# Performance work log

Hardware: AMD Instinct MI355X
Metric: run time of the kernel (lower is better)

The kernel has to match this reference:

```python
import jax, jax.numpy as jnp
import numpy as np

NIBBLES_PER_I32 = 8


def unpack_int4(q):
    """Unpack int32 [..., n] -> uint4 values in int32 [..., n*8], LSB-first."""
    shifts = (jnp.arange(NIBBLES_PER_I32, dtype=jnp.int32) * 4)
    nib = (q[..., None] >> shifts) & 0xF  # [..., n, 8]
    return nib.reshape(q.shape[:-1] + (q.shape[-1] * NIBBLES_PER_I32,))


def setup_inputs() -> dict:
    key = jax.random.key(0)
    k_x, k_w, k_z, k_s, k_b = jax.random.split(key, 5)
    B, S, IN, OUT, G = 2, 4096, 4096, 4096, 32
    x = jax.random.normal(k_x, (B, S, IN), dtype=jnp.float16)
    qweight = jax.random.randint(k_w, (OUT, IN // 8), 0, 2147483647, dtype=jnp.int32)
    qzeros = jax.random.randint(k_z, (G, OUT // 8), 0, 2147483647, dtype=jnp.int32)
    scales = (jax.random.uniform(k_s, (G, OUT), dtype=jnp.float32) * 0.01 + 0.001).astype(jnp.float16)
    bias = (jax.random.normal(k_b, (OUT,), dtype=jnp.float32) * 0.01).astype(jnp.float16)
    return {"x": x, "qweight": qweight, "qzeros": qzeros, "scales": scales, "bias": bias}


def reference(x, qweight, qzeros, scales, bias):
    # GPTQ W4A16: dequantize int4 weight with per-group scales/zero-points, then GEMM + bias.
    x = x.astype(jnp.float16)
    wq = unpack_int4(qweight)            # [out, in] int4 values
    zq = unpack_int4(qzeros)             # [groups, out]
    out_f, in_f = wq.shape
    G = scales.shape[0]
    gsize = in_f // G
    wq_g = wq.reshape(out_f, G, gsize)                       # [out, G, gsize]
    zero = zq.T.astype(jnp.float16)[:, :, None]              # [out, G, 1]
    scale = scales.T.astype(jnp.float16)[:, :, None]         # [out, G, 1]
    w = ((wq_g.astype(jnp.float16) - zero) * scale).reshape(out_f, in_f)  # [out, in] fp16
    y = jnp.einsum("bsi,oi->bso", x, w)                     # [B, S, out]
    return y + bias
```

## Files before the change

kernel.cpp:

```cpp
#include <hip/hip_runtime.h>
#include <cstdint>

typedef unsigned short u16;
typedef unsigned int   u32;
typedef unsigned long long u64;

typedef _Float16 f16x2 __attribute__((ext_vector_type(2)));
typedef _Float16 f16x8 __attribute__((ext_vector_type(8)));
typedef float    f32x4 __attribute__((ext_vector_type(4)));

__device__ __forceinline__ u32 cvt_pk(float a, float b) {
    return __builtin_bit_cast(u32, __builtin_amdgcn_cvt_pkrtz(a, b));
}

__device__ __forceinline__ f16x8 unpack_dq(u32 q, f16x2 cz, f16x2 cs) {
    const u32 b0 = (q & 0x000F000Fu) | 0x64006400u;
    const u32 b1 = ((q >> 4) & 0x000F000Fu) | 0x64006400u;
    const u32 b2 = ((q >> 8) & 0x000F000Fu) | 0x64006400u;
    const u32 b3 = ((q >> 12) & 0x000F000Fu) | 0x64006400u;
    const f16x2 w0 = (__builtin_bit_cast(f16x2, b0) - cz) * cs;
    const f16x2 w1 = (__builtin_bit_cast(f16x2, b1) - cz) * cs;
    const f16x2 w2 = (__builtin_bit_cast(f16x2, b2) - cz) * cs;
    const f16x2 w3 = (__builtin_bit_cast(f16x2, b3) - cz) * cs;
    uint4 w;
    w.x = __builtin_bit_cast(u32, w0);
    w.y = __builtin_bit_cast(u32, w1);
    w.z = __builtin_bit_cast(u32, w2);
    w.w = __builtin_bit_cast(u32, w3);
    return __builtin_bit_cast(f16x8, w);
}

__device__ __forceinline__ void load_lds16(const void* g, void* l) {
    __builtin_amdgcn_global_load_lds(
        (const __attribute__((address_space(1))) void*)g,
        (__attribute__((address_space(3))) void*)l,
        16, 0, 0);
}

__global__ __launch_bounds__(256) void gptq_prepass(
    const float* __restrict__ X, u16* __restrict__ Xh)
{
    const u32 tile = blockIdx.x;
    const u32 mt = tile >> 6, t = tile & 63;
    const float* bsrc = X + ((u64)mt << 19) + t * 64;
    u16* bdst = Xh + ((u64)tile << 13);
#pragma unroll
    for (int pass = 0; pass < 4; ++pass) {
        const u32 idx = pass * 256 + threadIdx.x;
        const u32 r = idx >> 3, sg = idx & 7, g = sg ^ (r & 7);
        const float* s = bsrc + ((u64)r << 12) + g * 8;
        const float4 f0 = *(const float4*)s;
        const float4 f1 = *(const float4*)(s + 4);
        uint4 w;
        w.x = cvt_pk(f0.x, f1.x);
        w.y = cvt_pk(f0.y, f1.y);
        w.z = cvt_pk(f0.z, f1.z);
        w.w = cvt_pk(f0.w, f1.w);
        *(uint4*)(bdst + idx * 8) = w;
    }
}

__global__ __launch_bounds__(256) void gptq_dequantB(
    const int* __restrict__ QW, const int* __restrict__ QZ,
    const float* __restrict__ SC, u16* __restrict__ Bt)
{
    __shared__ int tile[64][65];
    const u32 bkq = blockIdx.x;
    const u32 bn  = blockIdx.y;
    const u32 t = threadIdx.x;
    const u32 r = t >> 4, c4 = (t & 15) * 4;
#pragma unroll
    for (int p = 0; p < 4; ++p) {
        const u32 row = p * 16 + r;
        const int4 v = *(const int4*)(QW + (u64)(bn * 64 + row) * 512
                                         + bkq * 64 + c4);
        tile[row][c4 + 0] = v.x; tile[row][c4 + 1] = v.y;
        tile[row][c4 + 2] = v.z; tile[row][c4 + 3] = v.w;
    }
    __syncthreads();
    char* BtB = (char*)Bt;
#pragma unroll
    for (int p = 0; p < 4; ++p) {
        const u32 kql = p * 16 + r;
        const u32 chunk = bkq * 64 + kql;
        const u32 g = chunk >> 4;
        const u32 quad = chunk & 3;
        const u64 base = ((u64)((chunk >> 2) * 256)) * 1024 + quad * 256;
#pragma unroll
        for (int e = 0; e < 4; ++e) {
            const u32 n = bn * 64 + c4 + e;
            const u32 q = (u32)tile[c4 + e][kql];
            const float s = SC[g * 4096 + n];
            const int zw = QZ[g * 512 + (n >> 3)];
            const int z = (zw >> ((n & 7) * 4)) & 0xF;
            const _Float16 hs = (_Float16)s;
            const _Float16 hz = (_Float16)(float)(1024 + z);
            const f16x8 v = unpack_dq(q, (f16x2){hz, hz}, (f16x2){hs, hs});
            *(f16x8*)(BtB + base + (u64)(n >> 4) * 1024 + (n & 15) * 16) = v;
        }
    }
}

__global__ __launch_bounds__(256, 2) void gptq_gemm_dq(
    const u16* __restrict__ Xh,
    const u16* __restrict__ Bt,
    const float* __restrict__ BIAS,
    float* __restrict__ Y)
{
    constexpr int N = 4096, NT = 64;

    __shared__ __align__(16) u16 Alds[2][128 * 64];

    const int tid  = threadIdx.x;
    const int lane = tid & 63;
    const int wid  = tid >> 6;

    const int mt = blockIdx.x;
    const int m0 = mt * 128;
    const int n0 = blockIdx.y * 256;

    f32x4 acc[8][4];
#pragma unroll
    for (int i = 0; i < 8; i++)
#pragma unroll
        for (int j = 0; j < 4; j++)
            acc[i][j] = (f32x4){0.f, 0.f, 0.f, 0.f};

    const int fr   = lane & 15;
    const int quad = lane >> 4;
    const int fr7  = fr & 7;

    const char* xsrc = (const char*)Xh + (((u64)mt * NT) << 14)
                     + wid * 4096 + lane * 16;

    const int nb16 = (n0 >> 4) + wid * 4;
    const char* btb = (const char*)Bt + (u64)nb16 * 1024 + lane * 16;

    f16x8 bq[2][2][4];

    auto STAGE = [&](int buf, int t) {
        const char* s = xsrc + ((u64)t << 14);
        char* d = (char*)&Alds[buf][0] + wid * 4096;
#pragma unroll
        for (int i = 0; i < 4; i++)
            load_lds16(s + i * 1024, d + i * 1024);
    };

    auto FETCH_B = [&](int t, int nb) {
#pragma unroll
        for (int ks = 0; ks < 2; ks++) {
            const char* p = btb + ((u64)(t * 2 + ks) << 18);
#pragma unroll
            for (int ni = 0; ni < 4; ni++)
                bq[nb][ks][ni] = *(const f16x8*)(p + ni * 1024);
        }
    };

    auto COMPUTE = [&](int buf, int nb) {
#pragma unroll
        for (int ks = 0; ks < 2; ks++) {
            const int gsw = ((ks * 4 + quad) ^ fr7) * 8;
            __builtin_amdgcn_s_setprio(1);
#pragma unroll
            for (int mi = 0; mi < 8; mi++) {
                const f16x8 af =
                    *(const f16x8*)(&Alds[buf][(mi * 16 + fr) * 64 + gsw]);
#pragma unroll
                for (int ni = 0; ni < 4; ni++)
                    acc[mi][ni] = __builtin_amdgcn_mfma_f32_16x16x32_f16(
                        af, bq[nb][ks][ni], acc[mi][ni], 0, 0, 0);
            }
            __builtin_amdgcn_s_setprio(0);
        }
    };

    FETCH_B(0, 0);
    STAGE(0, 0);
    STAGE(1, 1);
    asm volatile("s_waitcnt vmcnt(4)\n\ts_barrier" ::: "memory");

    for (int t = 0; t <= 60; t += 2) {
        FETCH_B(t + 1, 1);
        COMPUTE(0, 0);
        asm volatile("s_barrier" ::: "memory");
        STAGE(0, t + 2);
        asm volatile("s_waitcnt vmcnt(12)\n\ts_barrier" ::: "memory");

        FETCH_B(t + 2, 0);
        COMPUTE(1, 1);
        asm volatile("s_barrier" ::: "memory");
        STAGE(1, t + 3);
        asm volatile("s_waitcnt vmcnt(12)\n\ts_barrier" ::: "memory");
    }

    FETCH_B(63, 1);
    COMPUTE(0, 0);
    asm volatile("s_waitcnt vmcnt(8)\n\ts_barrier" ::: "memory");
    COMPUTE(1, 1);

    const int cn  = lane & 15;
    const int q4r = quad * 4;
#pragma unroll
    for (int ni = 0; ni < 4; ni++) {
        const int col = n0 + wid * 64 + ni * 16 + cn;
        const float bz = BIAS[col];
#pragma unroll
        for (int mi = 0; mi < 8; mi++) {
            const int rbase = m0 + mi * 16 + q4r;
#pragma unroll
            for (int r = 0; r < 4; r++) {
                Y[(u64)(rbase + r) * N + col] = acc[mi][ni][r] + bz;
            }
        }
    }
}

__global__ __launch_bounds__(256) void gptq_transpose(
    const int* __restrict__ QW, int* __restrict__ QWt)
{
    __shared__ int tile[64][65];
    const u32 bkq = blockIdx.x, bn = blockIdx.y;
    const u32 t = threadIdx.x;
    const u32 r = t >> 4, c4 = (t & 15) * 4;
#pragma unroll
    for (int p = 0; p < 4; ++p) {
        const u32 row = p * 16 + r;
        const int4 v = *(const int4*)(QW + (u64)(bn * 64 + row) * 512
                                         + bkq * 64 + c4);
        tile[row][c4 + 0] = v.x; tile[row][c4 + 1] = v.y;
        tile[row][c4 + 2] = v.z; tile[row][c4 + 3] = v.w;
    }
    __syncthreads();
#pragma unroll
    for (int p = 0; p < 4; ++p) {
        const u32 kql = p * 16 + r;
        int4 v;
        v.x = tile[c4 + 0][kql]; v.y = tile[c4 + 1][kql];
        v.z = tile[c4 + 2][kql]; v.w = tile[c4 + 3][kql];
        *(int4*)(QWt + (u64)(bkq * 64 + kql) * 4096 + bn * 64 + c4) = v;
    }
}

__global__ __launch_bounds__(256, 2) void gptq_gemm_dma(
    const u16* __restrict__ Xh, const int* __restrict__ QWt,
    const int* __restrict__ QZ, const float* __restrict__ SC,
    const float* __restrict__ BIAS, float* __restrict__ Y)
{
    constexpr int N = 4096, NT = 64;
    __shared__ __align__(16) u16 Alds[2][128 * 64];
    const int tid = threadIdx.x, lane = tid & 63, wid = tid >> 6;
    const int mt = blockIdx.x, m0 = mt * 128, n0 = blockIdx.y * 256;
    f32x4 acc[8][4];
#pragma unroll
    for (int i = 0; i < 8; i++)
#pragma unroll
        for (int j = 0; j < 4; j++) acc[i][j] = (f32x4){0.f, 0.f, 0.f, 0.f};
    const int fr = lane & 15, quad = lane >> 4, fr7 = fr & 7;
    const char* xsrc = (const char*)Xh + (((u64)mt * NT) << 14)
                     + wid * 4096 + lane * 16;
    const int nbase = n0 + wid * 64 + fr;
    const char* QWtB = (const char*)QWt;
    const u64 qtbase = (u64)((u32)(quad * 4096 + nbase) * 4u);
    int bq[2][8];
    float sf_st[4];
    int zw_st[4];
    f16x2 cs[4], cz[4];
    const int zsh = fr7 * 4;
    auto STAGE = [&](int buf, int t) {
        const char* s = xsrc + ((u64)t << 14);
        char* d = (char*)&Alds[buf][0] + wid * 4096;
#pragma unroll
        for (int i = 0; i < 4; i++) load_lds16(s + i * 1024, d + i * 1024);
    };
    auto FETCH_B = [&](int t, int nb) {
        const char* p = QWtB + ((u64)t << 17) + qtbase;
#pragma unroll
        for (int ni = 0; ni < 4; ni++) {
            bq[nb][ni * 2 + 0] = *(const int*)(p + ni * 64);
            bq[nb][ni * 2 + 1] = *(const int*)(p + 65536 + ni * 64);
        }
    };
    auto FETCH_SZ = [&](int g) {
#pragma unroll
        for (int ni = 0; ni < 4; ni++) {
            sf_st[ni] = SC[g * N + nbase + ni * 16];
            zw_st[ni] = QZ[g * (N / 8) + ((nbase + ni * 16) >> 3)];
        }
    };
    auto CONV_SZ = [&]() {
#pragma unroll
        for (int ni = 0; ni < 4; ni++) {
            const int z = (zw_st[ni] >> zsh) & 0xF;
            const _Float16 hs = (_Float16)sf_st[ni];
            const _Float16 hz = (_Float16)(float)(1024 + z);
            cs[ni] = (f16x2){hs, hs};
            cz[ni] = (f16x2){hz, hz};
        }
    };
    auto COMPUTE = [&](int buf, int nb) {
#pragma unroll
        for (int ks = 0; ks < 2; ks++) {
            f16x8 bfr[4];
#pragma unroll
            for (int ni = 0; ni < 4; ni++)
                bfr[ni] = unpack_dq((u32)bq[nb][ni * 2 + ks], cz[ni], cs[ni]);
            const int gsw = ((ks * 4 + quad) ^ fr7) * 8;
            __builtin_amdgcn_s_setprio(1);
#pragma unroll
            for (int mi = 0; mi < 8; mi++) {
                const f16x8 af =
                    *(const f16x8*)(&Alds[buf][(mi * 16 + fr) * 64 + gsw]);
#pragma unroll
                for (int ni = 0; ni < 4; ni++)
                    acc[mi][ni] = __builtin_amdgcn_mfma_f32_16x16x32_f16(
                        af, bfr[ni], acc[mi][ni], 0, 0, 0);
            }
            __builtin_amdgcn_s_setprio(0);
        }
    };
    FETCH_B(0, 0);
    FETCH_SZ(0);
    STAGE(0, 0);
    STAGE(1, 1);
    CONV_SZ();
    asm volatile("s_waitcnt vmcnt(4)\n\ts_barrier" ::: "memory");
    for (int t = 0; t <= 60; t += 2) {
        FETCH_B(t + 1, 1);
        FETCH_SZ((t >> 1) + 1);
        COMPUTE(0, 0);
        asm volatile("s_barrier" ::: "memory");
        STAGE(0, t + 2);
        asm volatile("s_waitcnt vmcnt(20)\n\ts_barrier" ::: "memory");
        FETCH_B(t + 2, 0);
        COMPUTE(1, 1);
        CONV_SZ();
        asm volatile("s_barrier" ::: "memory");
        STAGE(1, t + 3);
        asm volatile("s_waitcnt vmcnt(12)\n\ts_barrier" ::: "memory");
    }
    FETCH_B(63, 1);
    COMPUTE(0, 0);
    asm volatile("s_waitcnt vmcnt(8)\n\ts_barrier" ::: "memory");
    COMPUTE(1, 1);
    const int cn = lane & 15, q4r = quad * 4;
#pragma unroll
    for (int ni = 0; ni < 4; ni++) {
        const int col = n0 + wid * 64 + ni * 16 + cn;
        const float bz = BIAS[col];
#pragma unroll
        for (int mi = 0; mi < 8; mi++) {
            const int rbase = m0 + mi * 16 + q4r;
#pragma unroll
            for (int r = 0; r < 4; r++)
                Y[(u64)(rbase + r) * N + col] = acc[mi][ni][r] + bz;
        }
    }
}

__global__ __launch_bounds__(256, 2) void gptq_gemm_fb(
    const float* __restrict__ X, const int* __restrict__ QW,
    const int* __restrict__ QZ, const float* __restrict__ SC,
    const float* __restrict__ BIAS, float* __restrict__ Y)
{
    constexpr int N = 4096, K = 4096, KB = 512, NT = 64;
    __shared__ __align__(16) u16 Alds[2][128 * 64];
    __shared__ __align__(16) u16 Blds[2][128 * 64];
    const int tid = threadIdx.x, lane = tid & 63, wid = tid >> 6;
    const int m0 = blockIdx.x * 128, n0 = blockIdx.y * 128;
    f32x4 acc[4][4];
#pragma unroll
    for (int i = 0; i < 4; i++)
#pragma unroll
        for (int j = 0; j < 4; j++) acc[i][j] = (f32x4){0.f, 0.f, 0.f, 0.f};
    const int wm = (wid >> 1) * 64, wn = (wid & 1) * 64;
    const int lrowA = tid >> 3;
    const float* gA = X + (u64)(m0 + lrowA) * K + (tid & 7) * 8;
    const int sA = ((tid & 7) ^ (lrowA & 7)) * 8;
    const int nl = tid >> 1, kq0 = (tid & 1) * 4;
    const int nglob = n0 + nl;
    const int* qrow = QW + (u64)nglob * KB;
    const int nl7 = nl & 7, zsh = (nglob & 7) * 4;
    const float* scp = SC + nglob;
    const int* qzp = QZ + (nglob >> 3);
    const int fr = lane & 15, quad = lane >> 4, fr7 = fr & 7;
    float4 af32[8];
    int4 q4;
    float sf;
    int zw;
    auto FETCH = [&](int t) {
        const int kt = t * 64;
#pragma unroll
        for (int i = 0; i < 4; i++) {
            const float* pa = gA + (u64)i * 32 * K + kt;
            af32[2 * i] = *(const float4*)pa;
            af32[2 * i + 1] = *(const float4*)(pa + 4);
        }
        q4 = *(const int4*)(qrow + (kt >> 3) + kq0);
        const int g = t >> 1;
        sf = scp[g * N];
        zw = qzp[g * (N / 8)];
    };
    auto STORE = [&](int buf) {
#pragma unroll
        for (int i = 0; i < 4; i++) {
            const float4 f0 = af32[2 * i], f1 = af32[2 * i + 1];
            uint4 w;
            w.x = cvt_pk(f0.x, f1.x); w.y = cvt_pk(f0.y, f1.y);
            w.z = cvt_pk(f0.z, f1.z); w.w = cvt_pk(f0.w, f1.w);
            *(uint4*)(&Alds[buf][(i * 32 + lrowA) * 64 + sA]) = w;
        }
        const int z = (zw >> zsh) & 0xF;
        const _Float16 hs = (_Float16)sf;
        const _Float16 hz = (_Float16)(float)(1024 + z);
        const f16x2 cs2 = {hs, hs}, cz2 = {hz, hz};
        const int qv[4] = {q4.x, q4.y, q4.z, q4.w};
#pragma unroll
        for (int c = 0; c < 4; c++) {
            const f16x8 wv = unpack_dq((u32)qv[c], cz2, cs2);
            const int gran = ((kq0 + c) ^ nl7) * 8;
            *(f16x8*)(&Blds[buf][nl * 64 + gran]) = wv;
        }
    };
    auto COMPUTE = [&](int buf) {
#pragma unroll
        for (int ks = 0; ks < 2; ks++) {
            const int gsw = ((ks * 4 + quad) ^ fr7) * 8;
            f16x8 af[4], bfr[4];
#pragma unroll
            for (int i = 0; i < 4; i++)
                af[i] = *(const f16x8*)(&Alds[buf][(wm + i * 16 + fr) * 64 + gsw]);
#pragma unroll
            for (int i = 0; i < 4; i++)
                bfr[i] = *(const f16x8*)(&Blds[buf][(wn + i * 16 + fr) * 64 + gsw]);
#pragma unroll
            for (int mi = 0; mi < 4; mi++)
#pragma unroll
                for (int ni = 0; ni < 4; ni++)
                    acc[mi][ni] = __builtin_amdgcn_mfma_f32_16x16x32_f16(
                        af[mi], bfr[ni], acc[mi][ni], 0, 0, 0);
        }
    };
    FETCH(0); STORE(0); __syncthreads();
#pragma unroll 2
    for (int t = 0; t < NT; ++t) {
        const int cur = t & 1;
        if (t + 1 < NT) FETCH(t + 1);
        COMPUTE(cur);
        if (t + 1 < NT) STORE(cur ^ 1);
        __syncthreads();
    }
    const int cn = lane & 15, q4r = quad * 4;
#pragma unroll
    for (int ni = 0; ni < 4; ni++) {
        const int col = n0 + wn + ni * 16 + cn;
        const float bz = BIAS[col];
#pragma unroll
        for (int mi = 0; mi < 4; mi++) {
            const int rbase = m0 + wm + mi * 16 + q4r;
#pragma unroll
            for (int r = 0; r < 4; r++)
                Y[(u64)(rbase + r) * N + col] = acc[mi][ni][r] + bz;
        }
    }
}

extern "C" void kernel_launch(void* const* d_in, const int* in_sizes, int n_in,
                              void* d_out, int out_size, void* d_ws, size_t ws_size,
                              hipStream_t stream) {
    const float* X    = (const float*)d_in[0];
    const int*   QW   = (const int*)d_in[1];
    const int*   QZ   = (const int*)d_in[2];
    const float* SC   = (const float*)d_in[3];
    const float* BIAS = (const float*)d_in[4];
    float* Y = (float*)d_out;

    const size_t needXh = (size_t)8192 * 4096 * sizeof(u16);
    const size_t needNew = needXh + (size_t)4096 * 4096 * 2;
    const size_t needMid = needXh + (size_t)512 * 4096 * 4;
    if (ws_size >= needNew) {
        u16* Xh = (u16*)d_ws;
        u16* Bt = (u16*)((char*)d_ws + needXh);
        gptq_prepass<<<4096, 256, 0, stream>>>(X, Xh);
        gptq_dequantB<<<dim3(8, 64), 256, 0, stream>>>(QW, QZ, SC, Bt);
        dim3 grid(64, 16, 1);
        gptq_gemm_dq<<<grid, 256, 0, stream>>>(Xh, Bt, BIAS, Y);
    } else if (ws_size >= needMid) {
        u16* Xh  = (u16*)d_ws;
        int* QWt = (int*)((char*)d_ws + needXh);
        gptq_prepass<<<4096, 256, 0, stream>>>(X, Xh);
        gptq_transpose<<<dim3(8, 64), 256, 0, stream>>>(QW, QWt);
        dim3 grid(64, 16, 1);
        gptq_gemm_dma<<<grid, 256, 0, stream>>>(Xh, QWt, QZ, SC, BIAS, Y);
    } else {
        dim3 grid(64, 32, 1);
        gptq_gemm_fb<<<grid, 256, 0, stream>>>(X, QW, QZ, SC, BIAS, Y);
    }
}
```

Baseline: 480.8 us.

## Deepen A-tile LDS pipeline to four stages with sched barriers

Grows the shared-memory A buffer from two to four stages and restructures the main loop so each step computes one stage while prefetching B two tiles ahead and staging A three tiles ahead. Scheduling barriers pin the order of compute, fetch and stage, and the vmcnt waits are relaxed so more global loads stay in flight. The aim is to hide global load latency better. In exchange LDS use doubles, which may limit occupancy. The tail iterations wrap indices modulo 64, so they issue redundant loads past the last tile.

```diff
diff --git a/kernel.cpp b/kernel.cpp
--- a/kernel.cpp
+++ b/kernel.cpp
@@ -109,7 +109,7 @@
 {
     constexpr int N = 4096, NT = 64;
 
-    __shared__ __align__(16) u16 Alds[2][128 * 64];
+    __shared__ __align__(16) u16 Alds[4][128 * 64];
 
     const int tid  = threadIdx.x;
     const int lane = tid & 63;
@@ -175,28 +175,55 @@
     };
 
     FETCH_B(0, 0);
+    FETCH_B(1, 1);
+    __builtin_amdgcn_sched_barrier(0);
     STAGE(0, 0);
     STAGE(1, 1);
-    asm volatile("s_waitcnt vmcnt(4)\n\ts_barrier" ::: "memory");
-
-    for (int t = 0; t <= 60; t += 2) {
-        FETCH_B(t + 1, 1);
-        COMPUTE(0, 0);
-        asm volatile("s_barrier" ::: "memory");
-        STAGE(0, t + 2);
-        asm volatile("s_waitcnt vmcnt(12)\n\ts_barrier" ::: "memory");
-
-        FETCH_B(t + 2, 0);
-        COMPUTE(1, 1);
-        asm volatile("s_barrier" ::: "memory");
-        STAGE(1, t + 3);
-        asm volatile("s_waitcnt vmcnt(12)\n\ts_barrier" ::: "memory");
-    }
-
-    FETCH_B(63, 1);
+    STAGE(2, 2);
+    __builtin_amdgcn_sched_barrier(0);
+    asm volatile("s_waitcnt vmcnt(8)\n\ts_barrier" ::: "memory");
+
     COMPUTE(0, 0);
-    asm volatile("s_waitcnt vmcnt(8)\n\ts_barrier" ::: "memory");
+    FETCH_B(2, 0);
+    __builtin_amdgcn_sched_barrier(0);
+    STAGE(3, 3);
+    __builtin_amdgcn_sched_barrier(0);
+    asm volatile("s_waitcnt vmcnt(16)\n\ts_barrier" ::: "memory");
+
     COMPUTE(1, 1);
+    FETCH_B(3, 1);
+    __builtin_amdgcn_sched_barrier(0);
+    STAGE(0, 4);
+    __builtin_amdgcn_sched_barrier(0);
+    asm volatile("s_waitcnt vmcnt(24)\n\ts_barrier" ::: "memory");
+
+    COMPUTE(2, 0);
+    FETCH_B(4, 0);
+    __builtin_amdgcn_sched_barrier(0);
+    STAGE(1, 5);
+    __builtin_amdgcn_sched_barrier(0);
+    asm volatile("s_waitcnt vmcnt(24)\n\ts_barrier" ::: "memory");
+
+    COMPUTE(3, 1);
+    FETCH_B(5, 1);
+    __builtin_amdgcn_sched_barrier(0);
+    STAGE(2, 6);
+    __builtin_amdgcn_sched_barrier(0);
+    asm volatile("s_waitcnt vmcnt(24)\n\ts_barrier" ::: "memory");
+
+    for (int tb = 1; tb < 16; ++tb) {
+        const int t0 = tb * 4;
+#pragma unroll
+        for (int p = 0; p < 4; ++p) {
+            const int t = t0 + p;
+            COMPUTE(p, p & 1);
+            FETCH_B((t + 2) & 63, p & 1);
+            __builtin_amdgcn_sched_barrier(0);
+            STAGE((p + 3) & 3, (t + 3) & 63);
+            __builtin_amdgcn_sched_barrier(0);
+            asm volatile("s_waitcnt vmcnt(24)\n\ts_barrier" ::: "memory");
+        }
+    }
 
     const int cn  = lane & 15;
     const int q4r = quad * 4;
```

After: 479.4 us. No clear change (-0.3%).

## Shrink GEMM block tile to 128x128 with 2x2 warp layout for higher occupancy

Applied to the files above, without the earlier changes.

Changes the dequantized-GEMM block tile from 128x256 to 128x128, splitting the four waves into a 2x2 grid of 64x64 sub-tiles instead of four 128x64 column strips. This halves the per-wave accumulator registers and allows three blocks per SM via launch bounds, and the grid doubles in N. B fragments are now prefetched one k-slice at a time, and the epilogue prologue/tail is folded into the loop with wrapped indices. The cost is lower A reuse per B load, more total A traffic, and redundant loads past the last tile.

```diff
diff --git a/kernel.cpp b/kernel.cpp
--- a/kernel.cpp
+++ b/kernel.cpp
@@ -101,7 +101,7 @@
     }
 }
 
-__global__ __launch_bounds__(256, 2) void gptq_gemm_dq(
+__global__ __launch_bounds__(256, 3) void gptq_gemm_dq(
     const u16* __restrict__ Xh,
     const u16* __restrict__ Bt,
     const float* __restrict__ BIAS,
@@ -117,11 +117,13 @@
 
     const int mt = blockIdx.x;
     const int m0 = mt * 128;
-    const int n0 = blockIdx.y * 256;
-
-    f32x4 acc[8][4];
-#pragma unroll
-    for (int i = 0; i < 8; i++)
+    const int n0 = blockIdx.y * 128;
+    const int wm = (wid >> 1) * 64;
+    const int wn = (wid & 1) * 64;
+
+    f32x4 acc[4][4];
+#pragma unroll
+    for (int i = 0; i < 4; i++)
 #pragma unroll
         for (int j = 0; j < 4; j++)
             acc[i][j] = (f32x4){0.f, 0.f, 0.f, 0.f};
@@ -133,10 +135,10 @@
     const char* xsrc = (const char*)Xh + (((u64)mt * NT) << 14)
                      + wid * 4096 + lane * 16;
 
-    const int nb16 = (n0 >> 4) + wid * 4;
+    const int nb16 = (n0 >> 4) + (wid & 1) * 4;
     const char* btb = (const char*)Bt + (u64)nb16 * 1024 + lane * 16;
 
-    f16x8 bq[2][2][4];
+    f16x8 bq[2][4];
 
     auto STAGE = [&](int buf, int t) {
         const char* s = xsrc + ((u64)t << 14);
@@ -146,67 +148,60 @@
             load_lds16(s + i * 1024, d + i * 1024);
     };
 
-    auto FETCH_B = [&](int t, int nb) {
-#pragma unroll
-        for (int ks = 0; ks < 2; ks++) {
-            const char* p = btb + ((u64)(t * 2 + ks) << 18);
+    auto FETCH_B_KS = [&](int t, int ks, int slot) {
+        const char* p = btb + ((u64)(t * 2 + ks) << 18);
+#pragma unroll
+        for (int ni = 0; ni < 4; ni++)
+            bq[slot][ni] = *(const f16x8*)(p + ni * 1024);
+    };
+
+    auto COMPUTE_KS = [&](int buf, int ks, int slot) {
+        const int gsw = ((ks * 4 + quad) ^ fr7) * 8;
+        __builtin_amdgcn_s_setprio(1);
+#pragma unroll
+        for (int mi = 0; mi < 4; mi++) {
+            const f16x8 af =
+                *(const f16x8*)(&Alds[buf][(wm + mi * 16 + fr) * 64 + gsw]);
 #pragma unroll
             for (int ni = 0; ni < 4; ni++)
-                bq[nb][ks][ni] = *(const f16x8*)(p + ni * 1024);
-        }
-    };
-
-    auto COMPUTE = [&](int buf, int nb) {
-#pragma unroll
-        for (int ks = 0; ks < 2; ks++) {
-            const int gsw = ((ks * 4 + quad) ^ fr7) * 8;
-            __builtin_amdgcn_s_setprio(1);
-#pragma unroll
-            for (int mi = 0; mi < 8; mi++) {
-                const f16x8 af =
-                    *(const f16x8*)(&Alds[buf][(mi * 16 + fr) * 64 + gsw]);
-#pragma unroll
-                for (int ni = 0; ni < 4; ni++)
-                    acc[mi][ni] = __builtin_amdgcn_mfma_f32_16x16x32_f16(
-                        af, bq[nb][ks][ni], acc[mi][ni], 0, 0, 0);
-            }
-            __builtin_amdgcn_s_setprio(0);
-        }
-    };
-
-    FETCH_B(0, 0);
+                acc[mi][ni] = __builtin_amdgcn_mfma_f32_16x16x32_f16(
+                    af, bq[slot][ni], acc[mi][ni], 0, 0, 0);
+        }
+        __builtin_amdgcn_s_setprio(0);
+    };
+
+    FETCH_B_KS(0, 0, 0);
     STAGE(0, 0);
     STAGE(1, 1);
     asm volatile("s_waitcnt vmcnt(4)\n\ts_barrier" ::: "memory");
 
-    for (int t = 0; t <= 60; t += 2) {
-        FETCH_B(t + 1, 1);
-        COMPUTE(0, 0);
+    for (int t = 0; t < NT; t += 2) {
+        FETCH_B_KS(t, 1, 1);
+        COMPUTE_KS(0, 0, 0);
+        FETCH_B_KS((t + 1) & 63, 0, 0);
+        COMPUTE_KS(0, 1, 1);
         asm volatile("s_barrier" ::: "memory");
-        STAGE(0, t + 2);
+        STAGE(0, (t + 2) & 63);
         asm volatile("s_waitcnt vmcnt(12)\n\ts_barrier" ::: "memory");
 
-        FETCH_B(t + 2, 0);
-        COMPUTE(1, 1);
+        FETCH_B_KS((t + 1) & 63, 1, 1);
+        COMPUTE_KS(1, 0, 0);
+        FETCH_B_KS((t + 2) & 63, 0, 0);
+        COMPUTE_KS(1, 1, 1);
         asm volatile("s_barrier" ::: "memory");
-        STAGE(1, t + 3);
+        STAGE(1, (t + 3) & 63);
         asm volatile("s_waitcnt vmcnt(12)\n\ts_barrier" ::: "memory");
     }
-
-    FETCH_B(63, 1);
-    COMPUTE(0, 0);
-    asm volatile("s_waitcnt vmcnt(8)\n\ts_barrier" ::: "memory");
-    COMPUTE(1, 1);
 
     const int cn  = lane & 15;
     const int q4r = quad * 4;
 #pragma unroll
     for (int ni = 0; ni < 4; ni++) {
-        const int col = n0 + wid * 64 + ni * 16 + cn;
+        const int col = n0 + wn + ni * 16 + cn;
         const float bz = BIAS[col];
 #pragma unroll
-        for (int mi = 0; mi < 8; mi++) {
-            const int rbase = m0 + mi * 16 + q4r;
+        for (int mi = 0; mi < 4; mi++) {
+            const int rbase = m0 + wm + mi * 16 + q4r;
 #pragma unroll
             for (int r = 0; r < 4; r++) {
                 Y[(u64)(rbase + r) * N + col] = acc[mi][ni][r] + bz;
@@ -482,7 +477,7 @@
         u16* Bt = (u16*)((char*)d_ws + needXh);
         gptq_prepass<<<4096, 256, 0, stream>>>(X, Xh);
         gptq_dequantB<<<dim3(8, 64), 256, 0, stream>>>(QW, QZ, SC, Bt);
-        dim3 grid(64, 16, 1);
+        dim3 grid(64, 32, 1);
         gptq_gemm_dq<<<grid, 256, 0, stream>>>(Xh, Bt, BIAS, Y);
     } else if (ws_size >= needMid) {
         u16* Xh  = (u16*)d_ws;
```

After: 507.8 us. 1.06x slower.

## Triple-buffer A tiles in GEMM and fuse the two prep kernels into one launch

Applied to the files above, without the earlier changes.

The GEMM moves from two to three LDS buffers for A. Each phase now issues the B fetch and the next A stage before computing on the current buffer, which removes the mid-iteration barrier and adds sched_barriers to keep the compiler from reordering across them. The activation conversion and the weight dequant kernels are merged into one launch using blockIdx ranges, saving a launch and letting both run concurrently. Three buffers raise LDS use per block, which may lower occupancy below the two blocks per SM requested in launch bounds.

```diff
diff --git a/kernel.cpp b/kernel.cpp
--- a/kernel.cpp
+++ b/kernel.cpp
@@ -37,66 +37,66 @@
         16, 0, 0);
 }
 
-__global__ __launch_bounds__(256) void gptq_prepass(
-    const float* __restrict__ X, u16* __restrict__ Xh)
-{
-    const u32 tile = blockIdx.x;
-    const u32 mt = tile >> 6, t = tile & 63;
-    const float* bsrc = X + ((u64)mt << 19) + t * 64;
-    u16* bdst = Xh + ((u64)tile << 13);
-#pragma unroll
-    for (int pass = 0; pass < 4; ++pass) {
-        const u32 idx = pass * 256 + threadIdx.x;
-        const u32 r = idx >> 3, sg = idx & 7, g = sg ^ (r & 7);
-        const float* s = bsrc + ((u64)r << 12) + g * 8;
-        const float4 f0 = *(const float4*)s;
-        const float4 f1 = *(const float4*)(s + 4);
-        uint4 w;
-        w.x = cvt_pk(f0.x, f1.x);
-        w.y = cvt_pk(f0.y, f1.y);
-        w.z = cvt_pk(f0.z, f1.z);
-        w.w = cvt_pk(f0.w, f1.w);
-        *(uint4*)(bdst + idx * 8) = w;
-    }
-}
-
-__global__ __launch_bounds__(256) void gptq_dequantB(
+__global__ __launch_bounds__(256) void gptq_prep_fused(
+    const float* __restrict__ X, u16* __restrict__ Xh,
     const int* __restrict__ QW, const int* __restrict__ QZ,
     const float* __restrict__ SC, u16* __restrict__ Bt)
 {
     __shared__ int tile[64][65];
-    const u32 bkq = blockIdx.x;
-    const u32 bn  = blockIdx.y;
-    const u32 t = threadIdx.x;
-    const u32 r = t >> 4, c4 = (t & 15) * 4;
-#pragma unroll
-    for (int p = 0; p < 4; ++p) {
-        const u32 row = p * 16 + r;
-        const int4 v = *(const int4*)(QW + (u64)(bn * 64 + row) * 512
-                                         + bkq * 64 + c4);
-        tile[row][c4 + 0] = v.x; tile[row][c4 + 1] = v.y;
-        tile[row][c4 + 2] = v.z; tile[row][c4 + 3] = v.w;
-    }
-    __syncthreads();
-    char* BtB = (char*)Bt;
-#pragma unroll
-    for (int p = 0; p < 4; ++p) {
-        const u32 kql = p * 16 + r;
-        const u32 chunk = bkq * 64 + kql;
-        const u32 g = chunk >> 4;
-        const u32 quad = chunk & 3;
-        const u64 base = ((u64)((chunk >> 2) * 256)) * 1024 + quad * 256;
-#pragma unroll
-        for (int e = 0; e < 4; ++e) {
-            const u32 n = bn * 64 + c4 + e;
-            const u32 q = (u32)tile[c4 + e][kql];
-            const float s = SC[g * 4096 + n];
-            const int zw = QZ[g * 512 + (n >> 3)];
-            const int z = (zw >> ((n & 7) * 4)) & 0xF;
-            const _Float16 hs = (_Float16)s;
-            const _Float16 hz = (_Float16)(float)(1024 + z);
-            const f16x8 v = unpack_dq(q, (f16x2){hz, hz}, (f16x2){hs, hs});
-            *(f16x8*)(BtB + base + (u64)(n >> 4) * 1024 + (n & 15) * 16) = v;
+    if (blockIdx.x < 4096) {
+        const u32 tl = blockIdx.x;
+        const u32 mt = tl >> 6, t = tl & 63;
+        const float* bsrc = X + ((u64)mt << 19) + t * 64;
+        u16* bdst = Xh + ((u64)tl << 13);
+#pragma unroll
+        for (int pass = 0; pass < 4; ++pass) {
+            const u32 idx = pass * 256 + threadIdx.x;
+            const u32 r = idx >> 3, sg = idx & 7, g = sg ^ (r & 7);
+            const float* s = bsrc + ((u64)r << 12) + g * 8;
+            const float4 f0 = *(const float4*)s;
+            const float4 f1 = *(const float4*)(s + 4);
+            uint4 w;
+            w.x = cvt_pk(f0.x, f1.x);
+            w.y = cvt_pk(f0.y, f1.y);
+            w.z = cvt_pk(f0.z, f1.z);
+            w.w = cvt_pk(f0.w, f1.w);
+            *(uint4*)(bdst + idx * 8) = w;
+        }
+    } else {
+        const u32 bid = blockIdx.x - 4096;
+        const u32 bkq = bid >> 6;
+        const u32 bn  = bid & 63;
+        const u32 t = threadIdx.x;
+        const u32 r = t >> 4, c4 = (t & 15) * 4;
+#pragma unroll
+        for (int p = 0; p < 4; ++p) {
+            const u32 row = p * 16 + r;
+            const int4 v = *(const int4*)(QW + (u64)(bn * 64 + row) * 512
+                                             + bkq * 64 + c4);
+            tile[row][c4 + 0] = v.x; tile[row][c4 + 1] = v.y;
+            tile[row][c4 + 2] = v.z; tile[row][c4 + 3] = v.w;
+        }
+        __syncthreads();
+        char* BtB = (char*)Bt;
+#pragma unroll
+        for (int p = 0; p < 4; ++p) {
+            const u32 kql = p * 16 + r;
+            const u32 chunk = bkq * 64 + kql;
+            const u32 g = chunk >> 4;
+            const u32 quad = chunk & 3;
+            const u64 base = ((u64)((chunk >> 2) * 256)) * 1024 + quad * 256;
+#pragma unroll
+            for (int e = 0; e < 4; ++e) {
+                const u32 n = bn * 64 + c4 + e;
+                const u32 q = (u32)tile[c4 + e][kql];
+                const float s = SC[g * 4096 + n];
+                const int zw = QZ[g * 512 + (n >> 3)];
+                const int z = (zw >> ((n & 7) * 4)) & 0xF;
+                const _Float16 hs = (_Float16)s;
+                const _Float16 hz = (_Float16)(float)(1024 + z);
+                const f16x8 v = unpack_dq(q, (f16x2){hz, hz}, (f16x2){hs, hs});
+                *(f16x8*)(BtB + base + (u64)(n >> 4) * 1024 + (n & 15) * 16) = v;
+            }
         }
     }
 }
@@ -109,7 +109,7 @@
 {
     constexpr int N = 4096, NT = 64;
 
-    __shared__ __align__(16) u16 Alds[2][128 * 64];
+    __shared__ __align__(16) u16 Alds[3][128 * 64];
 
     const int tid  = threadIdx.x;
     const int lane = tid & 63;
@@ -174,29 +174,35 @@
         }
     };
 
+    auto PHASE = [&](int bufc, int bufs, int sc, int sn, int tn, int ts) {
+        FETCH_B(tn, sn);
+        __builtin_amdgcn_sched_barrier(0);
+        STAGE(bufs, ts);
+        __builtin_amdgcn_sched_barrier(0);
+        COMPUTE(bufc, sc);
+        asm volatile("s_waitcnt vmcnt(12)\n\ts_barrier" ::: "memory");
+    };
+
     FETCH_B(0, 0);
+    __builtin_amdgcn_sched_barrier(0);
     STAGE(0, 0);
     STAGE(1, 1);
+    __builtin_amdgcn_sched_barrier(0);
     asm volatile("s_waitcnt vmcnt(4)\n\ts_barrier" ::: "memory");
 
-    for (int t = 0; t <= 60; t += 2) {
-        FETCH_B(t + 1, 1);
-        COMPUTE(0, 0);
-        asm volatile("s_barrier" ::: "memory");
-        STAGE(0, t + 2);
-        asm volatile("s_waitcnt vmcnt(12)\n\ts_barrier" ::: "memory");
-
-        FETCH_B(t + 2, 0);
-        COMPUTE(1, 1);
-        asm volatile("s_barrier" ::: "memory");
-        STAGE(1, t + 3);
-        asm volatile("s_waitcnt vmcnt(12)\n\ts_barrier" ::: "memory");
-    }
-
-    FETCH_B(63, 1);
-    COMPUTE(0, 0);
-    asm volatile("s_waitcnt vmcnt(8)\n\ts_barrier" ::: "memory");
-    COMPUTE(1, 1);
+    for (int t0 = 0; t0 < 60; t0 += 6) {
+        PHASE(0, 2, 0, 1, t0 + 1, t0 + 2);
+        PHASE(1, 0, 1, 0, t0 + 2, t0 + 3);
+        PHASE(2, 1, 0, 1, t0 + 3, t0 + 4);
+        PHASE(0, 2, 1, 0, t0 + 4, t0 + 5);
+        PHASE(1, 0, 0, 1, t0 + 5, t0 + 6);
+        PHASE(2, 1, 1, 0, t0 + 6, t0 + 7);
+    }
+
+    PHASE(0, 2, 0, 1, 61, 62);
+    PHASE(1, 0, 1, 0, 62, 63);
+    PHASE(2, 1, 0, 1, 63, 0);
+    COMPUTE(0, 1);
 
     const int cn  = lane & 15;
     const int q4r = quad * 4;
@@ -480,14 +486,14 @@
     if (ws_size >= needNew) {
         u16* Xh = (u16*)d_ws;
         u16* Bt = (u16*)((char*)d_ws + needXh);
-        gptq_prepass<<<4096, 256, 0, stream>>>(X, Xh);
-        gptq_dequantB<<<dim3(8, 64), 256, 0, stream>>>(QW, QZ, SC, Bt);
+        gptq_prep_fused<<<4608, 256, 0, stream>>>(X, Xh, QW, QZ, SC, Bt);
         dim3 grid(64, 16, 1);
         gptq_gemm_dq<<<grid, 256, 0, stream>>>(Xh, Bt, BIAS, Y);
     } else if (ws_size >= needMid) {
         u16* Xh  = (u16*)d_ws;
         int* QWt = (int*)((char*)d_ws + needXh);
-        gptq_prepass<<<4096, 256, 0, stream>>>(X, Xh);
+        gptq_prep_fused<<<4096, 256, 0, stream>>>(X, Xh, QW, QZ, SC,
+                                                  (u16*)nullptr);
         gptq_transpose<<<dim3(8, 64), 256, 0, stream>>>(QW, QWt);
         dim3 grid(64, 16, 1);
         gptq_gemm_dma<<<grid, 256, 0, stream>>>(Xh, QWt, QZ, SC, BIAS, Y);
```

After: 476.8 us. Within noise of the previous version (-0.8%).
